# Optimization experiments

Measured on AMD Instinct MI355X. Metric: run time of the kernel, lower is better.

The kernel has to match this reference:

```python
import jax, jax.numpy as jnp
import numpy as np

B, C_IN, N = 8, 512, 4096   # batch, input channels, timesteps
D, K = 256, 2048            # code dim (n_out), codebook size (vq_n_embed)
EMA_G = 0.99                # vq_ema_gamma


def setup_inputs() -> dict:
    key = jax.random.key(0)
    k1, k2, k3 = jax.random.split(key, 3)
    z = jax.random.normal(k1, (B, C_IN, N), jnp.float32)
    # emb: xavier_uniform with gain=10 over (K, D)
    eb = 10.0 * np.sqrt(6.0 / (K + D))
    emb = jax.random.uniform(k2, (K, D), jnp.float32, -eb, eb)
    # 1x1 Conv1d weight (no bias), xavier_uniform over (D, C_IN)
    wb = np.sqrt(6.0 / (D + C_IN))
    W = jax.random.uniform(k3, (D, C_IN), jnp.float32, -wb, wb)
    # EMA buffers as initialized in __init__
    ema_numer = emb * (1.0 - EMA_G)
    ema_denom = jnp.ones((K,), jnp.float32) * (1.0 - EMA_G)
    return {"z": z, "W": W, "emb": emb, "ema_numer": ema_numer, "ema_denom": ema_denom}


def reference(z, W, emb, ema_numer, ema_denom):
    # 1x1 conv (no bias): ze (B, D, N)
    ze = jnp.einsum('dc,bcn->bdn', W, z)
    e = jax.lax.stop_gradient(emb)  # sg(emb)
    # Squared L2 distances (B, K, N) via ||ze||^2 + ||e||^2 - 2 e.ze
    # (mathematically equal to the broadcasted (ze-e)^2 sum, without the
    #  huge (B,K,D,N) intermediate)
    ze_sq = jnp.sum(ze * ze, axis=1)              # (B, N)
    e_sq = jnp.sum(e * e, axis=1)                 # (K,)
    cross = jnp.einsum('kd,bdn->bkn', e, ze)      # (B, K, N)
    d2 = ze_sq[:, None, :] + e_sq[None, :, None] - 2.0 * cross
    min_ind = jnp.argmin(d2, axis=1)              # (B, N) int
    zq = jnp.take(e, min_ind, axis=0).transpose(0, 2, 1)  # (B, D, N)
    # ReplaceGrad straight-through: value = zq, gradient flows to ze
    out = ze + jax.lax.stop_gradient(zq - ze)
    # EMA codebook statistics (scatter-add over assignments)
    flat_ind = min_ind.reshape(-1)                          # (B*N,)
    flat_ze = ze.transpose(0, 2, 1).reshape(-1, D)          # (B*N, D)
    z_sum = jax.ops.segment_sum(flat_ze, flat_ind, num_segments=K)
    n_sum = jax.ops.segment_sum(jnp.ones((flat_ind.shape[0],), ze.dtype), flat_ind, num_segments=K)
    ema_numer_new = EMA_G * ema_numer + (1.0 - EMA_G) * z_sum
    ema_denom_new = EMA_G * ema_denom + (1.0 - EMA_G) * n_sum
    return out, ema_numer_new, ema_denom_new
```

## Files before the change

### kernel.cpp

```cpp
#include <hip/hip_runtime.h>

#define B_   8
#define CIN  512
#define NN_  4096
#define DD   256
#define KK   2048
#define KSPLIT 4
#define KPER (KK / KSPLIT)
#define NG   (B_ * NN_)

typedef _Float16 f16x8 __attribute__((ext_vector_type(8)));
typedef _Float16 f16x4 __attribute__((ext_vector_type(4)));
typedef float    f32x16 __attribute__((ext_vector_type(16)));

#define MFMA16 __builtin_amdgcn_mfma_f32_32x32x16_f16

#define GLDS16(gp, lp) __builtin_amdgcn_global_load_lds( \
    (const __attribute__((address_space(1))) void*)(gp), \
    (__attribute__((address_space(3))) void*)(lp), 16, 0, 0)

__global__ __launch_bounds__(256) void k_esq(const float* __restrict__ emb,
                                             float* __restrict__ esq,
                                             _Float16* __restrict__ emb_h,
                                             _Float16* __restrict__ emb_l) {
  int t = threadIdx.x;
  int lane = t & 63;
  int k = blockIdx.x * 4 + (t >> 6);
  float4 v = *(const float4*)&emb[(size_t)k * DD + 4 * lane];
  float s = v.x * v.x + v.y * v.y + v.z * v.z + v.w * v.w;
  f16x4 h, l;
  float* vp = (float*)&v;
#pragma unroll
  for (int i = 0; i < 4; i++) {
    _Float16 hh = (_Float16)vp[i];
    h[i] = hh;
    l[i] = (_Float16)(vp[i] - (float)hh);
  }
  *(f16x4*)&emb_h[(size_t)k * DD + 4 * lane] = h;
  *(f16x4*)&emb_l[(size_t)k * DD + 4 * lane] = l;
  for (int off = 32; off > 0; off >>= 1) s += __shfl_down(s, off, 64);
  if (lane == 0) esq[k] = s;
}

__global__ __launch_bounds__(256) void k_ze(const float* __restrict__ W,
                                            const float* __restrict__ z,
                                            _Float16* __restrict__ zeT_h,
                                            _Float16* __restrict__ zeT_l) {
  __shared__ __align__(16) char sm[67584];
  const int t = threadIdx.x;
  const int w = t >> 6, lane = t & 63;
  const int lr = lane & 31, lh = lane >> 5;
  const int wm = w & 1, wn = w >> 1;
  const int swz = (lr >> 1) & 3;
  const int b = blockIdx.z, d0 = blockIdx.y * 128, n0 = blockIdx.x * 128;
  const float* zb = z + (size_t)b * CIN * NN_ + n0;

  _Float16* Ah = (_Float16*)sm;
  _Float16* Al = (_Float16*)(sm + 16384);
  float*    Zs = (float*)(sm + 32768);

  auto stageA = [&](int buf, int c0) {
#pragma unroll
    for (int i = 0; i < 4; i++) {
      int fid = i * 256 + t;
      int d = fid >> 3, q8 = fid & 7;
      float4 v = *(const float4*)&W[(size_t)(d0 + d) * CIN + c0 + 4 * q8];
      float* vp = (float*)&v;
      f16x4 h, l;
#pragma unroll
      for (int e = 0; e < 4; e++) {
        _Float16 hh = (_Float16)vp[e];
        h[e] = hh;
        l[e] = (_Float16)(vp[e] - (float)hh);
      }
      int p16 = (q8 >> 1) ^ ((d >> 1) & 3);
      int off = (buf * 128 + d) * 32 + p16 * 8 + (q8 & 1) * 4;
      *(f16x4*)&Ah[off] = h;
      *(f16x4*)&Al[off] = l;
    }
  };
  auto stageZ = [&](int buf, int c0) {
#pragma unroll
    for (int i = 0; i < 4; i++) {
      int r = 8 * w + 2 * i;
      float* lbase = Zs + (size_t)buf * 4096 + r * 128;
      const float* gp = zb + (size_t)(c0 + r + lh) * NN_ + 4 * lr;
      GLDS16(gp, lbase);
    }
  };

  f32x16 acc[2][2];
#pragma unroll
  for (int mt = 0; mt < 2; mt++)
#pragma unroll
    for (int nt = 0; nt < 2; nt++)
#pragma unroll
      for (int i = 0; i < 16; i++) acc[mt][nt][i] = 0.0f;

  stageA(0, 0);
  stageZ(0, 0);
  int buf = 0;
  for (int c0 = 0; c0 < CIN; c0 += 32) {
    __syncthreads();
    if (c0 + 32 < CIN) { stageA(buf ^ 1, c0 + 32); stageZ(buf ^ 1, c0 + 32); }
    const _Float16* AhB = Ah + (size_t)buf * 128 * 32;
    const _Float16* AlB = Al + (size_t)buf * 128 * 32;
    const float*    ZsB = Zs + (size_t)buf * 4096;
#pragma unroll
    for (int s = 0; s < 2; s++) {
      const int cbase = 16 * s + 8 * lh;
      const int pa = (2 * s + lh) ^ swz;
      const int aoff = pa * 8;
      f16x8 ah0 = *(const f16x8*)&AhB[(wm * 64 + lr) * 32 + aoff];
      f16x8 ah1 = *(const f16x8*)&AhB[(wm * 64 + 32 + lr) * 32 + aoff];
      f16x8 al0 = *(const f16x8*)&AlB[(wm * 64 + lr) * 32 + aoff];
      f16x8 al1 = *(const f16x8*)&AlB[(wm * 64 + 32 + lr) * 32 + aoff];
      f16x8 bh0, bl0, bh1, bl1;
#pragma unroll
      for (int j = 0; j < 8; j++) {
        float x0 = ZsB[(cbase + j) * 128 + wn * 64 + lr];
        float x1 = ZsB[(cbase + j) * 128 + wn * 64 + 32 + lr];
        _Float16 h0 = (_Float16)x0;
        bh0[j] = h0;
        bl0[j] = (_Float16)(x0 - (float)h0);
        _Float16 h1 = (_Float16)x1;
        bh1[j] = h1;
        bl1[j] = (_Float16)(x1 - (float)h1);
      }
      acc[0][0] = MFMA16(ah0, bh0, acc[0][0], 0, 0, 0);
      acc[0][1] = MFMA16(ah0, bh1, acc[0][1], 0, 0, 0);
      acc[1][0] = MFMA16(ah1, bh0, acc[1][0], 0, 0, 0);
      acc[1][1] = MFMA16(ah1, bh1, acc[1][1], 0, 0, 0);
      acc[0][0] = MFMA16(ah0, bl0, acc[0][0], 0, 0, 0);
      acc[0][1] = MFMA16(ah0, bl1, acc[0][1], 0, 0, 0);
      acc[1][0] = MFMA16(ah1, bl0, acc[1][0], 0, 0, 0);
      acc[1][1] = MFMA16(ah1, bl1, acc[1][1], 0, 0, 0);
      acc[0][0] = MFMA16(al0, bh0, acc[0][0], 0, 0, 0);
      acc[0][1] = MFMA16(al0, bh1, acc[0][1], 0, 0, 0);
      acc[1][0] = MFMA16(al1, bh0, acc[1][0], 0, 0, 0);
      acc[1][1] = MFMA16(al1, bh1, acc[1][1], 0, 0, 0);
    }
    buf ^= 1;
  }

  __syncthreads();
  _Float16* Eh = (_Float16*)sm;
  _Float16* El = (_Float16*)(sm + 33792);
#pragma unroll
  for (int mt = 0; mt < 2; mt++)
#pragma unroll
    for (int nt = 0; nt < 2; nt++) {
      int n_l = wn * 64 + nt * 32 + lr;
#pragma unroll
      for (int g = 0; g < 4; g++) {
        int d_l = wm * 64 + mt * 32 + 8 * g + 4 * lh;
        f16x4 h, l;
#pragma unroll
        for (int e = 0; e < 4; e++) {
          float x = acc[mt][nt][4 * g + e];
          _Float16 hh = (_Float16)x;
          h[e] = hh;
          l[e] = (_Float16)(x - (float)hh);
        }
        *(f16x4*)&Eh[n_l * 132 + d_l] = h;
        *(f16x4*)&El[n_l * 132 + d_l] = l;
      }
    }
  __syncthreads();
  _Float16* gh = zeT_h + ((size_t)b * NN_ + n0) * DD + d0;
  _Float16* gl = zeT_l + ((size_t)b * NN_ + n0) * DD + d0;
#pragma unroll
  for (int i = 0; i < 16; i++) {
    int n = i * 8 + w * 2 + lh;
    int d = 4 * lr;
    *(f16x4*)&gh[(size_t)n * DD + d] = *(const f16x4*)&Eh[n * 132 + d];
    *(f16x4*)&gl[(size_t)n * DD + d] = *(const f16x4*)&El[n * 132 + d];
  }
}

__global__ __launch_bounds__(256) void k_argmin(const _Float16* __restrict__ emb_h,
                                                const _Float16* __restrict__ emb_l,
                                                const _Float16* __restrict__ zeT_h,
                                                const _Float16* __restrict__ zeT_l,
                                                const float* __restrict__ esq,
                                                float* __restrict__ pval,
                                                int* __restrict__ pidx) {
  __shared__ __align__(16) char sm[36864];
  const int t = threadIdx.x;
  const int w = t >> 6, lane = t & 63;
  const int lr = lane & 31, lh = lane >> 5;
  const int wm = w & 1, wn = w >> 1;
  const int swz = (lr >> 1) & 3;
  const int b = blockIdx.y, n0 = blockIdx.x * 128, ks = blockIdx.z;
  const int kbase = ks * KPER;

  float* esqs = (float*)(sm + 32768);
  *(float2*)&esqs[2 * t] = *(const float2*)&esq[kbase + 2 * t];

  const _Float16* zb_h = zeT_h + ((size_t)b * NN_ + n0) * DD;
  const _Float16* zb_l = zeT_l + ((size_t)b * NN_ + n0) * DD;
  const _Float16* pB0h = zb_h + (size_t)(wn * 64 + lr) * DD + 8 * lh;
  const _Float16* pB1h = pB0h + 32 * DD;
  const _Float16* pB0l = zb_l + (size_t)(wn * 64 + lr) * DD + 8 * lh;
  const _Float16* pB1l = pB0l + 32 * DD;

  auto stageE = [&](int buf, int kt, int dc) {
    const int k0 = kbase + kt * 128;
    const int q = lane & 3, rr = lane >> 2;
    const int g = q ^ ((rr >> 1) & 3);
    const int rb0 = 32 * w;
#pragma unroll
    for (int j = 0; j < 2; j++) {
      int rb = rb0 + 16 * j;
      int r = rb + rr;
      size_t eo = (size_t)(k0 + r) * DD + dc + 8 * g;
      char* lb = sm + (size_t)buf * 8192 + rb * 64;
      GLDS16(emb_h + eo, lb);
      GLDS16(emb_l + eo, lb + 16384);
    }
  };
  auto loadB = [&](f16x8* bh, f16x8* bl, int dc) {
#pragma unroll
    for (int s = 0; s < 2; s++) {
      bh[2 * s + 0] = *(const f16x8*)(pB0h + dc + 16 * s);
      bh[2 * s + 1] = *(const f16x8*)(pB1h + dc + 16 * s);
      bl[2 * s + 0] = *(const f16x8*)(pB0l + dc + 16 * s);
      bl[2 * s + 1] = *(const f16x8*)(pB1l + dc + 16 * s);
    }
  };

  f32x16 vzero;
#pragma unroll
  for (int i = 0; i < 16; i++) vzero[i] = 0.0f;

  float bestv[2];
  int   besti[2];
  bestv[0] = bestv[1] = 3.4e38f;
  besti[0] = besti[1] = 0;

  f16x8 B0h[4], B0l[4], B1h[4], B1l[4];

  stageE(0, 0, 0);
  loadB(B0h, B0l, 0);
  for (int kt = 0; kt < 4; kt++) {
    f32x16 acc00 = vzero, acc01 = vzero, acc10 = vzero, acc11 = vzero;
#pragma unroll
    for (int i = 0; i < 8; i++) {
      const int dc = i * 32;
      const int cbuf = i & 1;
      __syncthreads();
      if (dc + 32 < DD) {
        stageE(cbuf ^ 1, kt, dc + 32);
        loadB(cbuf ? B0h : B1h, cbuf ? B0l : B1l, dc + 32);
      } else if (kt < 3) {
        stageE(cbuf ^ 1, kt + 1, 0);
        loadB(cbuf ? B0h : B1h, cbuf ? B0l : B1l, 0);
      }
      const _Float16* EHb = (const _Float16*)(sm + cbuf * 8192);
      const _Float16* ELb = (const _Float16*)(sm + 16384 + cbuf * 8192);
      const f16x8* bhc = cbuf ? B1h : B0h;
      const f16x8* blc = cbuf ? B1l : B0l;
#pragma unroll
      for (int s = 0; s < 2; s++) {
        const int pa = (2 * s + lh) ^ swz;
        const int ar0 = (wm * 64 + lr) * 32 + pa * 8;
        const int ar1 = (wm * 64 + 32 + lr) * 32 + pa * 8;
        f16x8 ah0 = *(const f16x8*)(EHb + ar0);
        f16x8 ah1 = *(const f16x8*)(EHb + ar1);
        f16x8 al0 = *(const f16x8*)(ELb + ar0);
        f16x8 al1 = *(const f16x8*)(ELb + ar1);
        f16x8 bh0 = bhc[2 * s + 0], bh1 = bhc[2 * s + 1];
        f16x8 bl0 = blc[2 * s + 0], bl1 = blc[2 * s + 1];
        acc00 = MFMA16(ah0, bh0, acc00, 0, 0, 0);
        acc01 = MFMA16(ah0, bh1, acc01, 0, 0, 0);
        acc10 = MFMA16(ah1, bh0, acc10, 0, 0, 0);
        acc11 = MFMA16(ah1, bh1, acc11, 0, 0, 0);
        acc00 = MFMA16(ah0, bl0, acc00, 0, 0, 0);
        acc01 = MFMA16(ah0, bl1, acc01, 0, 0, 0);
        acc10 = MFMA16(ah1, bl0, acc10, 0, 0, 0);
        acc11 = MFMA16(ah1, bl1, acc11, 0, 0, 0);
        acc00 = MFMA16(al0, bh0, acc00, 0, 0, 0);
        acc01 = MFMA16(al0, bh1, acc01, 0, 0, 0);
        acc10 = MFMA16(al1, bh0, acc10, 0, 0, 0);
        acc11 = MFMA16(al1, bh1, acc11, 0, 0, 0);
      }
    }
#pragma unroll
    for (int mt = 0; mt < 2; mt++)
#pragma unroll
      for (int nt = 0; nt < 2; nt++) {
        const f32x16& a = (mt == 0) ? (nt == 0 ? acc00 : acc01)
                                    : (nt == 0 ? acc10 : acc11);
#pragma unroll
        for (int r = 0; r < 16; r++) {
          int kl = kt * 128 + wm * 64 + mt * 32 + (r & 3) + 8 * (r >> 2) + 4 * lh;
          float d2 = esqs[kl] - 2.0f * a[r];
          int kg = kbase + kl;
          if (d2 < bestv[nt] || (d2 == bestv[nt] && kg < besti[nt])) {
            bestv[nt] = d2; besti[nt] = kg;
          }
        }
      }
  }

#pragma unroll
  for (int nt = 0; nt < 2; nt++) {
    float ov = __shfl_xor(bestv[nt], 32, 64);
    int   oi = __shfl_xor(besti[nt], 32, 64);
    if (ov < bestv[nt] || (ov == bestv[nt] && oi < besti[nt])) {
      bestv[nt] = ov; besti[nt] = oi;
    }
  }
  float* pv = (float*)(sm + 34816);
  int*   pi = (int*)(sm + 35840);
  __syncthreads();
  if (lh == 0) {
#pragma unroll
    for (int nt = 0; nt < 2; nt++) {
      pv[(w * 2 + nt) * 32 + lr] = bestv[nt];
      pi[(w * 2 + nt) * 32 + lr] = besti[nt];
    }
  }
  __syncthreads();
  if (t < 128) {
    int wn2 = t >> 6, nt = (t >> 5) & 1, nl = t & 31;
    int i0 = ((2 * wn2 + 0) * 2 + nt) * 32 + nl;
    int i1 = ((2 * wn2 + 1) * 2 + nt) * 32 + nl;
    float v0 = pv[i0], v1 = pv[i1];
    int   j0 = pi[i0], j1 = pi[i1];
    if (v1 < v0 || (v1 == v0 && j1 < j0)) { v0 = v1; j0 = j1; }
    size_t o = ((size_t)ks * B_ + b) * NN_ + n0 + t;
    pval[o] = v0;
    pidx[o] = j0;
  }
}

__global__ __launch_bounds__(256) void k_histm(const float* __restrict__ pval,
                                               const int* __restrict__ pidx,
                                               int* __restrict__ mind,
                                               int* __restrict__ hist) {
  __shared__ int h[KK];
  const int t = threadIdx.x;
#pragma unroll
  for (int i = 0; i < 8; i++) h[t + 256 * i] = 0;
  __syncthreads();
  const int base = blockIdx.x * 2048;
#pragma unroll
  for (int i = 0; i < 8; i++) {
    int g = base + i * 256 + t;
    float bv = pval[g];
    int   bi = pidx[g];
#pragma unroll
    for (int ks = 1; ks < KSPLIT; ks++) {
      float v = pval[(size_t)ks * NG + g];
      int  ii = pidx[(size_t)ks * NG + g];
      if (v < bv || (v == bv && ii < bi)) { bv = v; bi = ii; }
    }
    mind[g] = bi;
    atomicAdd(&h[bi], 1);
  }
  __syncthreads();
#pragma unroll
  for (int i = 0; i < 8; i++) {
    int v = h[t + 256 * i];
    if (v) atomicAdd(&hist[t + 256 * i], v);
  }
}

__global__ __launch_bounds__(256) void k_scan(const int* __restrict__ hist,
                                              int* __restrict__ cursor,
                                              float* __restrict__ nsumf) {
  __shared__ int ps[256];
  const int t = threadIdx.x;
  int c[8], s = 0;
#pragma unroll
  for (int e = 0; e < 8; e++) { c[e] = hist[8 * t + e]; s += c[e]; }
  ps[t] = s;
  __syncthreads();
  for (int off = 1; off < 256; off <<= 1) {
    int v = (t >= off) ? ps[t - off] : 0;
    __syncthreads();
    ps[t] += v;
    __syncthreads();
  }
  int run = ps[t] - s;
#pragma unroll
  for (int e = 0; e < 8; e++) {
    cursor[8 * t + e] = run;
    nsumf[8 * t + e] = (float)c[e];
    run += c[e];
  }
}

__global__ __launch_bounds__(256) void k_pos(const int* __restrict__ mind,
                                             int* __restrict__ cursor,
                                             int* __restrict__ sortp) {
  int g = blockIdx.x * 256 + threadIdx.x;
  int k = mind[g];
  int p = atomicAdd(&cursor[k], 1);
  sortp[p] = (k << 15) | g;
}

__global__ __launch_bounds__(256) void k_out(const float* __restrict__ emb,
                                             const int* __restrict__ mind,
                                             float* __restrict__ out) {
  __shared__ __align__(16) float E[64][257];
  __shared__ int idxl[64];
  const int t = threadIdx.x;
  const int b  = blockIdx.y;
  const int n0 = blockIdx.x * 64;
  if (t < 64) idxl[t] = mind[(size_t)b * NN_ + n0 + t];
  __syncthreads();

  for (int i = 0; i < 16; i++) {
    int cid = t + 256 * i;
    int r = cid >> 6, q = cid & 63;
    float4 v = *(const float4*)&emb[(size_t)idxl[r] * DD + 4 * q];
    float* vp = (float*)&v;
    E[r][4 * q + 0] = vp[0];
    E[r][4 * q + 1] = vp[1];
    E[r][4 * q + 2] = vp[2];
    E[r][4 * q + 3] = vp[3];
  }
  __syncthreads();
  const int nq = t & 15, dg = t >> 4;
  float* outb = out + (size_t)b * DD * NN_ + n0;
#pragma unroll
  for (int i = 0; i < 16; i++) {
    int d = i * 16 + dg;
    float4 v = make_float4(E[4 * nq + 0][d], E[4 * nq + 1][d],
                           E[4 * nq + 2][d], E[4 * nq + 3][d]);
    *(float4*)&outb[(size_t)d * NN_ + 4 * nq] = v;
  }
}

__global__ __launch_bounds__(256) void k_zsum(const int* __restrict__ sortp,
                                              const _Float16* __restrict__ zeT_h,
                                              const _Float16* __restrict__ zeT_l,
                                              float* __restrict__ z_sum) {
  __shared__ int sg[256];
  const int t = threadIdx.x;
  const int w = t >> 6, lane = t & 63;
  sg[t] = sortp[blockIdx.x * 256 + t];
  __syncthreads();
  const int base = w * 64;
  float acc[4] = {0.f, 0.f, 0.f, 0.f};
  int cur = sg[base] >> 15;
  for (int j = 0; j < 64; j++) {
    int e = sg[base + j];
    int k = e >> 15, g = e & 32767;
    if (k != cur) {
      float* zs = &z_sum[(size_t)cur * DD + 4 * lane];
#pragma unroll
      for (int x = 0; x < 4; x++) { atomicAdd(&zs[x], acc[x]); acc[x] = 0.f; }
      cur = k;
    }
    f16x4 h = *(const f16x4*)&zeT_h[(size_t)g * DD + 4 * lane];
    f16x4 l = *(const f16x4*)&zeT_l[(size_t)g * DD + 4 * lane];
#pragma unroll
    for (int x = 0; x < 4; x++) acc[x] += (float)h[x] + (float)l[x];
  }
  float* zs = &z_sum[(size_t)cur * DD + 4 * lane];
#pragma unroll
  for (int x = 0; x < 4; x++) atomicAdd(&zs[x], acc[x]);
}

__global__ __launch_bounds__(256) void k_ema(const float* __restrict__ ema_numer,
                                             const float* __restrict__ ema_denom,
                                             const float* __restrict__ z_sum,
                                             const float* __restrict__ nsumf,
                                             float* __restrict__ out_numer,
                                             float* __restrict__ out_denom) {
  const float G  = 0.99f;
  const float OG = 0.009999999776482582f;
  int i = blockIdx.x * 256 + threadIdx.x;
  if (i < KK * DD) {
    out_numer[i] = G * ema_numer[i] + OG * z_sum[i];
  } else {
    int j = i - KK * DD;
    if (j < KK) out_denom[j] = G * ema_denom[j] + OG * nsumf[j];
  }
}

extern "C" void kernel_launch(void* const* d_in, const int* in_sizes, int n_in,
                              void* d_out, int out_size, void* d_ws, size_t ws_size,
                              hipStream_t stream) {
  (void)in_sizes; (void)n_in; (void)out_size; (void)ws_size;
  const float* z         = (const float*)d_in[0];
  const float* W         = (const float*)d_in[1];
  const float* emb       = (const float*)d_in[2];
  const float* ema_numer = (const float*)d_in[3];
  const float* ema_denom = (const float*)d_in[4];

  float* out       = (float*)d_out;
  float* out_numer = out + (size_t)B_ * DD * NN_;
  float* out_denom = out_numer + (size_t)KK * DD;

  const size_t ZET = (size_t)B_ * NN_ * DD;
  _Float16* zeT_h = (_Float16*)d_ws;
  _Float16* zeT_l = zeT_h + ZET;
  float* esq    = (float*)(zeT_l + ZET);
  float* zsum   = esq + KK;
  int*   hist   = (int*)(zsum + (size_t)KK * DD);
  int*   cursor = hist + KK;
  float* nsumf  = (float*)(cursor + KK);
  float* pval   = nsumf + KK;
  int*   pidx   = (int*)(pval + (size_t)KSPLIT * NG);
  int*   mind   = pidx + (size_t)KSPLIT * NG;
  int*   sortp  = mind + NG;
  _Float16* emb_h = (_Float16*)(sortp + NG);
  _Float16* emb_l = emb_h + (size_t)KK * DD;

  hipMemsetAsync(zsum, 0, (size_t)(KK * DD + KK) * sizeof(float), stream);

  k_esq<<<dim3(KK / 4), 256, 0, stream>>>(emb, esq, emb_h, emb_l);
  k_ze<<<dim3(NN_ / 128, DD / 128, B_), 256, 0, stream>>>(W, z, zeT_h, zeT_l);
  k_argmin<<<dim3(NN_ / 128, B_, KSPLIT), 256, 0, stream>>>(emb_h, emb_l, zeT_h, zeT_l,
                                                            esq, pval, pidx);
  k_histm<<<dim3(NG / 2048), 256, 0, stream>>>(pval, pidx, mind, hist);
  k_scan<<<dim3(1), 256, 0, stream>>>(hist, cursor, nsumf);
  k_pos<<<dim3(NG / 256), 256, 0, stream>>>(mind, cursor, sortp);
  k_out<<<dim3(NN_ / 64, B_), 256, 0, stream>>>(emb, mind, out);
  k_zsum<<<dim3(NG / 256), 256, 0, stream>>>(sortp, zeT_h, zeT_l, zsum);
  k_ema<<<dim3((KK * DD + KK) / 256), 256, 0, stream>>>(ema_numer, ema_denom, zsum, nsumf,
                                                        out_numer, out_denom);
}
```

Before: 337.4 us.

## Drop register double-buffering of zeT operands and raise argmin occupancy

The argmin kernel stops prefetching the next zeT (B operand) fragments into a second register set. It now loads them from global memory at the start of each d-chunk, right before the MFMAs, and the d-loop is no longer unrolled. Launch bounds now request 3 blocks per CU, which lowers register pressure so more waves can hide latency. In exchange, global load latency for the B operand is exposed inside each iteration and has to be hidden by the extra occupancy.

```diff
diff --git a/kernel.cpp b/kernel.cpp
--- a/kernel.cpp
+++ b/kernel.cpp
@@ -178,13 +178,13 @@
   }
 }
 
-__global__ __launch_bounds__(256) void k_argmin(const _Float16* __restrict__ emb_h,
-                                                const _Float16* __restrict__ emb_l,
-                                                const _Float16* __restrict__ zeT_h,
-                                                const _Float16* __restrict__ zeT_l,
-                                                const float* __restrict__ esq,
-                                                float* __restrict__ pval,
-                                                int* __restrict__ pidx) {
+__global__ __launch_bounds__(256, 3) void k_argmin(const _Float16* __restrict__ emb_h,
+                                                   const _Float16* __restrict__ emb_l,
+                                                   const _Float16* __restrict__ zeT_h,
+                                                   const _Float16* __restrict__ zeT_l,
+                                                   const float* __restrict__ esq,
+                                                   float* __restrict__ pval,
+                                                   int* __restrict__ pidx) {
   __shared__ __align__(16) char sm[36864];
   const int t = threadIdx.x;
   const int w = t >> 6, lane = t & 63;
@@ -197,11 +197,10 @@
   float* esqs = (float*)(sm + 32768);
   *(float2*)&esqs[2 * t] = *(const float2*)&esq[kbase + 2 * t];
 
-  const _Float16* zb_h = zeT_h + ((size_t)b * NN_ + n0) * DD;
-  const _Float16* zb_l = zeT_l + ((size_t)b * NN_ + n0) * DD;
-  const _Float16* pB0h = zb_h + (size_t)(wn * 64 + lr) * DD + 8 * lh;
+  const size_t zrow = ((size_t)b * NN_ + n0 + wn * 64 + lr) * DD + 8 * lh;
+  const _Float16* pB0h = zeT_h + zrow;
   const _Float16* pB1h = pB0h + 32 * DD;
-  const _Float16* pB0l = zb_l + (size_t)(wn * 64 + lr) * DD + 8 * lh;
+  const _Float16* pB0l = zeT_l + zrow;
   const _Float16* pB1l = pB0l + 32 * DD;
 
   auto stageE = [&](int buf, int kt, int dc) {
@@ -219,15 +218,6 @@
       GLDS16(emb_l + eo, lb + 16384);
     }
   };
-  auto loadB = [&](f16x8* bh, f16x8* bl, int dc) {
-#pragma unroll
-    for (int s = 0; s < 2; s++) {
-      bh[2 * s + 0] = *(const f16x8*)(pB0h + dc + 16 * s);
-      bh[2 * s + 1] = *(const f16x8*)(pB1h + dc + 16 * s);
-      bl[2 * s + 0] = *(const f16x8*)(pB0l + dc + 16 * s);
-      bl[2 * s + 1] = *(const f16x8*)(pB1l + dc + 16 * s);
-    }
-  };
 
   f32x16 vzero;
 #pragma unroll
@@ -238,28 +228,24 @@
   bestv[0] = bestv[1] = 3.4e38f;
   besti[0] = besti[1] = 0;
 
-  f16x8 B0h[4], B0l[4], B1h[4], B1l[4];
-
   stageE(0, 0, 0);
-  loadB(B0h, B0l, 0);
+  int buf = 0;
   for (int kt = 0; kt < 4; kt++) {
     f32x16 acc00 = vzero, acc01 = vzero, acc10 = vzero, acc11 = vzero;
-#pragma unroll
-    for (int i = 0; i < 8; i++) {
-      const int dc = i * 32;
-      const int cbuf = i & 1;
+    for (int dc = 0; dc < DD; dc += 32) {
       __syncthreads();
-      if (dc + 32 < DD) {
-        stageE(cbuf ^ 1, kt, dc + 32);
-        loadB(cbuf ? B0h : B1h, cbuf ? B0l : B1l, dc + 32);
-      } else if (kt < 3) {
-        stageE(cbuf ^ 1, kt + 1, 0);
-        loadB(cbuf ? B0h : B1h, cbuf ? B0l : B1l, 0);
+      if (dc + 32 < DD) stageE(buf ^ 1, kt, dc + 32);
+      else if (kt < 3) stageE(buf ^ 1, kt + 1, 0);
+      f16x8 bh0[2], bh1[2], bl0[2], bl1[2];
+#pragma unroll
+      for (int s = 0; s < 2; s++) {
+        bh0[s] = *(const f16x8*)(pB0h + dc + 16 * s);
+        bh1[s] = *(const f16x8*)(pB1h + dc + 16 * s);
+        bl0[s] = *(const f16x8*)(pB0l + dc + 16 * s);
+        bl1[s] = *(const f16x8*)(pB1l + dc + 16 * s);
       }
-      const _Float16* EHb = (const _Float16*)(sm + cbuf * 8192);
-      const _Float16* ELb = (const _Float16*)(sm + 16384 + cbuf * 8192);
-      const f16x8* bhc = cbuf ? B1h : B0h;
-      const f16x8* blc = cbuf ? B1l : B0l;
+      const _Float16* EHb = (const _Float16*)(sm + buf * 8192);
+      const _Float16* ELb = (const _Float16*)(sm + 16384 + buf * 8192);
 #pragma unroll
       for (int s = 0; s < 2; s++) {
         const int pa = (2 * s + lh) ^ swz;
@@ -269,21 +255,20 @@
         f16x8 ah1 = *(const f16x8*)(EHb + ar1);
         f16x8 al0 = *(const f16x8*)(ELb + ar0);
         f16x8 al1 = *(const f16x8*)(ELb + ar1);
-        f16x8 bh0 = bhc[2 * s + 0], bh1 = bhc[2 * s + 1];
-        f16x8 bl0 = blc[2 * s + 0], bl1 = blc[2 * s + 1];
-        acc00 = MFMA16(ah0, bh0, acc00, 0, 0, 0);
-        acc01 = MFMA16(ah0, bh1, acc01, 0, 0, 0);
-        acc10 = MFMA16(ah1, bh0, acc10, 0, 0, 0);
-        acc11 = MFMA16(ah1, bh1, acc11, 0, 0, 0);
-        acc00 = MFMA16(ah0, bl0, acc00, 0, 0, 0);
-        acc01 = MFMA16(ah0, bl1, acc01, 0, 0, 0);
-        acc10 = MFMA16(ah1, bl0, acc10, 0, 0, 0);
-        acc11 = MFMA16(ah1, bl1, acc11, 0, 0, 0);
-        acc00 = MFMA16(al0, bh0, acc00, 0, 0, 0);
-        acc01 = MFMA16(al0, bh1, acc01, 0, 0, 0);
-        acc10 = MFMA16(al1, bh0, acc10, 0, 0, 0);
-        acc11 = MFMA16(al1, bh1, acc11, 0, 0, 0);
+        acc00 = MFMA16(ah0, bh0[s], acc00, 0, 0, 0);
+        acc01 = MFMA16(ah0, bh1[s], acc01, 0, 0, 0);
+        acc10 = MFMA16(ah1, bh0[s], acc10, 0, 0, 0);
+        acc11 = MFMA16(ah1, bh1[s], acc11, 0, 0, 0);
+        acc00 = MFMA16(ah0, bl0[s], acc00, 0, 0, 0);
+        acc01 = MFMA16(ah0, bl1[s], acc01, 0, 0, 0);
+        acc10 = MFMA16(ah1, bl0[s], acc10, 0, 0, 0);
+        acc11 = MFMA16(ah1, bl1[s], acc11, 0, 0, 0);
+        acc00 = MFMA16(al0, bh0[s], acc00, 0, 0, 0);
+        acc01 = MFMA16(al0, bh1[s], acc01, 0, 0, 0);
+        acc10 = MFMA16(al1, bh0[s], acc10, 0, 0, 0);
+        acc11 = MFMA16(al1, bh1[s], acc11, 0, 0, 0);
       }
+      buf ^= 1;
     }
 #pragma unroll
     for (int mt = 0; mt < 2; mt++)
```

After: 470.3 us. 39.4% more time.
